# Kernel tuning notes

Hardware: AMD Instinct MI355X
Metric: run time of the kernel (lower is better)

## Reference

```python
import jax, jax.numpy as jnp
import numpy as np

B, F, H, OUT, S = 32768, 256, 128, 64, 6
RELAX, EPS, BN_EPS = 1.5, 1e-05, 1e-05
SQRT_HALF = 0.7071067811865476


def _bn(h, g, b):
    # training-mode BatchNorm1d: biased batch statistics over dim 0
    m = h.mean(axis=0)
    v = h.var(axis=0)
    return (h - m) * jax.lax.rsqrt(v + BN_EPS) * g + b


def _tfrm(x, W, g, b, glu_act=True):
    h = _bn(x @ W, g, b)
    if glu_act:
        d = h.shape[1] // 2
        h = h[:, :d] * jax.nn.sigmoid(h[:, d:])
    return h


def setup_inputs() -> dict:
    key = jax.random.key(0)
    ks = jax.random.split(key, 6)
    f32 = jnp.float32
    return {
        "x": jax.random.normal(ks[0], (B, F), f32),
        "enc_g": jnp.ones((F,), f32), "enc_b": jnp.zeros((F,), f32),
        "W1": jax.random.normal(ks[1], (F, 2 * H), f32) * 0.05,
        "g1": jnp.ones((2 * H,), f32), "b1": jnp.zeros((2 * H,), f32),
        "W2": jax.random.normal(ks[2], (H, 2 * H), f32) * 0.05,
        "g2": jnp.ones((2 * H,), f32), "b2": jnp.zeros((2 * H,), f32),
        "W3": jax.random.normal(ks[3], (S, H, 2 * H), f32) * 0.05,
        "g3": jnp.ones((S, 2 * H), f32), "b3": jnp.zeros((S, 2 * H), f32),
        "W4": jax.random.normal(ks[4], (S, H, 2 * H), f32) * 0.05,
        "g4": jnp.ones((S, 2 * H), f32), "b4": jnp.zeros((S, 2 * H), f32),
        "Wc": jax.random.normal(ks[5], (S - 1, OUT, F), f32) * 0.05,
        "gc": jnp.ones((S - 1, F), f32), "bc": jnp.zeros((S - 1, F), f32),
    }


def reference(x, enc_g, enc_b, W1, g1, b1, W2, g2, b2, W3, g3, b3,
              W4, g4, b4, Wc, gc, bc):
    x = _bn(x, enc_g, enc_b)                      # [B, F]
    masked = x
    compl = jnp.ones((x.shape[0], F), x.dtype)    # complementary aggregated mask
    agg_out, agg_entropy = [], []
    for ni in range(S):
        h = _tfrm(masked, W1, g1, b1)                             # [B, H]
        h = (_tfrm(h, W2, g2, b2) + h) * SQRT_HALF
        h = (_tfrm(h, W3[ni], g3[ni], b3[ni]) + h) * SQRT_HALF
        h = (_tfrm(h, W4[ni], g4[ni], b4[ni]) + h) * SQRT_HALF
        if ni > 0:
            # NOTE: source uses x (not h) here -- replicated faithfully
            agg_out.append(jax.nn.relu(x[:, :OUT]))
        fc = h[:, OUT:]                                           # [B, OUT]
        if ni < S - 1:
            coef = _tfrm(fc, Wc[ni], gc[ni], bc[ni], glu_act=False)  # [B, F]
            mask_values = jax.nn.softmax(coef * compl, axis=1)
            compl = compl * (RELAX - mask_values)
            agg_entropy.append(
                jnp.mean(jnp.sum(-mask_values * jnp.log(mask_values + EPS), axis=1))
                / (S - 1))
            masked = mask_values * x
    out = jnp.sum(jnp.stack(agg_out, axis=0), axis=0)   # [B, OUT]
    entropy = jnp.sum(jnp.stack(agg_entropy))           # scalar
    return (out, entropy)
```

## Files before the change

kernel.cpp:

```cpp
#include <hip/hip_runtime.h>
#include <math.h>

#define BSZ   32768
#define FDIM  256
#define HDIM  128
#define OUTD  64
#define SQRT_HALF 0.70710678118654752f
#define BN_EPS 1e-5f
#define SM_EPS 1e-5f
#define INV_B (1.0f / 32768.0f)
#define NCPY  8
#define SLOT  (NCPY * 512)

typedef __attribute__((ext_vector_type(8))) short bf16x8;
typedef __attribute__((ext_vector_type(4))) float f32x4;

__device__ __forceinline__ float b2f(unsigned short u) {
    return __uint_as_float(((unsigned int)u) << 16);
}
__device__ __forceinline__ unsigned short f2b(float f) {
    unsigned int u = __float_as_uint(f);
    u += 0x7fff + ((u >> 16) & 1);
    return (unsigned short)(u >> 16);
}

__device__ __forceinline__ void async16(const void* g, void* l) {
    __builtin_amdgcn_global_load_lds(
        (const __attribute__((address_space(1))) void*)(uintptr_t)g,
        (__attribute__((address_space(3))) void*)(unsigned int)(uintptr_t)l,
        16, 0, 0);
}

__device__ inline float waveMaxAll(float v) {
#pragma unroll
    for (int m = 32; m > 0; m >>= 1) v = fmaxf(v, __shfl_xor(v, m, 64));
    return v;
}
__device__ inline float waveSumAll(float v) {
#pragma unroll
    for (int m = 32; m > 0; m >>= 1) v += __shfl_xor(v, m, 64);
    return v;
}

__global__ __launch_bounds__(256) void prep_w(
    const float* __restrict__ W1, const float* __restrict__ W2,
    const float* __restrict__ W3, const float* __restrict__ W4,
    const float* __restrict__ Wc,
    unsigned short* __restrict__ W1t, unsigned short* __restrict__ W2t,
    unsigned short* __restrict__ W3t, unsigned short* __restrict__ W4t,
    unsigned short* __restrict__ Wct)
{
    const int m = blockIdx.x, kz = blockIdx.y, n = threadIdx.x;
    const float* src; unsigned short* dst; int K;
    if (m == 0)      { src = W1;                        dst = W1t;               K = 256; }
    else if (m == 1) { src = W2;                        dst = W2t;               K = 128; }
    else if (m < 7)  { int i = m - 2;  src = W3 + (size_t)i * 128 * 256; dst = W3t + (size_t)i * 32768; K = 128; }
    else if (m < 12) { int i = m - 7;  src = W4 + (size_t)i * 128 * 256; dst = W4t + (size_t)i * 32768; K = 128; }
    else             { int i = m - 12; src = Wc + (size_t)i * 64 * 256;  dst = Wct + (size_t)i * 16384; K = 64; }
    const int k0 = kz * 32;
    if (k0 >= K) return;
    for (int k = k0; k < k0 + 32; ++k)
        dst[(size_t)n * K + k] = f2b(src[(size_t)k * 256 + n]);
}

__global__ __launch_bounds__(256) void colstats(const float* __restrict__ X,
                                                float* __restrict__ st0) {
    __shared__ float red[4][512];
    const int sub = threadIdx.x >> 6;
    const int c4  = (threadIdx.x & 63) << 2;
    float s[4] = {0.f, 0.f, 0.f, 0.f}, q[4] = {0.f, 0.f, 0.f, 0.f};
#pragma unroll 8
    for (int i = 0; i < 32; ++i) {
        const int row = blockIdx.x * 128 + i * 4 + sub;
        float4 v = *(const float4*)(X + (size_t)row * 256 + c4);
        s[0] += v.x; q[0] += v.x * v.x;
        s[1] += v.y; q[1] += v.y * v.y;
        s[2] += v.z; q[2] += v.z * v.z;
        s[3] += v.w; q[3] += v.w * v.w;
    }
#pragma unroll
    for (int e = 0; e < 4; ++e) {
        red[sub][c4 + e] = s[e];
        red[sub][256 + c4 + e] = q[e];
    }
    __syncthreads();
    const int t = threadIdx.x;
    const int cp = (blockIdx.x & (NCPY - 1)) * 512;
    float sS = red[0][t] + red[1][t] + red[2][t] + red[3][t];
    float sQ = red[0][256 + t] + red[1][256 + t] + red[2][256 + t] + red[3][256 + t];
    atomicAdd(&st0[cp + t], sS);
    atomicAdd(&st0[cp + 256 + t], sQ);
}

__global__ __launch_bounds__(256) void norm_x(const float* __restrict__ x,
                                              const float* __restrict__ st0,
                                              const float* __restrict__ g,
                                              const float* __restrict__ b,
                                              unsigned short* __restrict__ xb,
                                              float* __restrict__ out) {
    const int i4 = blockIdx.x * 256 + threadIdx.x;
    const int row = i4 >> 6, c4 = (i4 & 63) << 2;
    float4 xv = *(const float4*)(x + (size_t)row * 256 + c4);
    float sS[4] = {0.f, 0.f, 0.f, 0.f}, sQ[4] = {0.f, 0.f, 0.f, 0.f};
#pragma unroll
    for (int cp = 0; cp < NCPY; ++cp) {
        float4 a = *(const float4*)&st0[cp * 512 + c4];
        float4 q = *(const float4*)&st0[cp * 512 + 256 + c4];
        sS[0] += a.x; sS[1] += a.y; sS[2] += a.z; sS[3] += a.w;
        sQ[0] += q.x; sQ[1] += q.y; sQ[2] += q.z; sQ[3] += q.w;
    }
    float4 gv = *(const float4*)&g[c4];
    float4 bv = *(const float4*)&b[c4];
    const float* xp = (const float*)&xv;
    const float* gp = (const float*)&gv; const float* bp = (const float*)&bv;
    float n[4];
    ushort4 ob;
    unsigned short* obp = (unsigned short*)&ob;
#pragma unroll
    for (int e = 0; e < 4; ++e) {
        float mean = sS[e] * INV_B;
        float var  = sQ[e] * INV_B - mean * mean;
        float sc   = gp[e] * rsqrtf(var + BN_EPS);
        float sh   = bp[e] - mean * sc;
        n[e] = xp[e] * sc + sh;
        obp[e] = f2b(n[e]);
    }
    *(ushort4*)(xb + (size_t)row * 256 + c4) = ob;
    if (c4 < OUTD) {
        float4 ov = make_float4(5.0f * fmaxf(n[0], 0.f), 5.0f * fmaxf(n[1], 0.f),
                                5.0f * fmaxf(n[2], 0.f), 5.0f * fmaxf(n[3], 0.f));
        *(float4*)(out + (size_t)row * OUTD + c4) = ov;
    }
}

__device__ __forceinline__ void gemm_epilogue(
    f32x4 (&acc)[4][4], int row0, int wave, int lane, int tid, int bcp,
    float* redS, float* redQ,
    unsigned short* __restrict__ Pout, float* __restrict__ statsOut)
{
    const int fm = lane & 15;
    const int orow = row0 + (lane >> 4) * 4;
    const int ocol = wave * 64 + fm;
#pragma unroll
    for (int i = 0; i < 4; ++i)
#pragma unroll
        for (int j = 0; j < 4; ++j)
#pragma unroll
            for (int r = 0; r < 4; ++r)
                Pout[(size_t)(orow + i * 16 + r) * 256 + (ocol + j * 16)] = f2b(acc[i][j][r]);

#pragma unroll
    for (int j = 0; j < 4; ++j) {
        float s = 0.f, q = 0.f;
#pragma unroll
        for (int i = 0; i < 4; ++i)
#pragma unroll
            for (int r = 0; r < 4; ++r) {
                float v = acc[i][j][r];
                s += v; q += v * v;
            }
        s += __shfl_xor(s, 16, 64); s += __shfl_xor(s, 32, 64);
        q += __shfl_xor(q, 16, 64); q += __shfl_xor(q, 32, 64);
        if (lane < 16) {
            redS[wave * 64 + j * 16 + lane] = s;
            redQ[wave * 64 + j * 16 + lane] = q;
        }
    }
    __syncthreads();
    atomicAdd(&statsOut[bcp + tid], redS[tid]);
    atomicAdd(&statsOut[bcp + 256 + tid], redQ[tid]);
}

__global__ __launch_bounds__(256) void gemm_bf16(
    const unsigned short* __restrict__ A,
    const unsigned short* __restrict__ Wt, int K,
    unsigned short* __restrict__ P,
    float* __restrict__ statsOut)
{
    __shared__ short As[64 * 32];
    __shared__ short Bs[256 * 32];
    __shared__ float redS[256], redQ[256];

    const int tid  = threadIdx.x;
    const int wave = tid >> 6;
    const int lane = tid & 63;
    const int row0 = blockIdx.x * 64;
    const int bcp  = (blockIdx.x & (NCPY - 1)) * 512;

    const int sr = lane >> 2;
    const int sc = (lane & 3) * 8;
    const int fm = lane & 15;
    const int fq = (lane >> 4) * 8;

    f32x4 acc[4][4];
#pragma unroll
    for (int i = 0; i < 4; ++i)
#pragma unroll
        for (int j = 0; j < 4; ++j)
            acc[i][j] = (f32x4){0.f, 0.f, 0.f, 0.f};

    for (int k0 = 0; k0 < K; k0 += 32) {
        async16(A + (size_t)(row0 + wave * 16 + sr) * K + k0 + sc,
                (void*)(As + wave * 512 + lane * 8));
#pragma unroll
        for (int t = 0; t < 4; ++t) {
            const int wr = wave * 64 + t * 16 + sr;
            async16(Wt + (size_t)wr * K + k0 + sc,
                    (void*)(Bs + (wave * 4 + t) * 512 + lane * 8));
        }
        __syncthreads();

        bf16x8 af[4], bfr[4];
#pragma unroll
        for (int i = 0; i < 4; ++i)
            af[i] = *(const bf16x8*)(As + (i * 16 + fm) * 32 + fq);
#pragma unroll
        for (int j = 0; j < 4; ++j)
            bfr[j] = *(const bf16x8*)(Bs + (wave * 64 + j * 16 + fm) * 32 + fq);
#pragma unroll
        for (int i = 0; i < 4; ++i)
#pragma unroll
            for (int j = 0; j < 4; ++j)
                acc[i][j] = __builtin_amdgcn_mfma_f32_16x16x32_bf16(af[i], bfr[j], acc[i][j], 0, 0, 0);
        __syncthreads();
    }

    gemm_epilogue(acc, row0, wave, lane, tid, bcp, redS, redQ, P, statsOut);
}

template <bool RES, bool WRITE_H>
__global__ __launch_bounds__(256) void gemm_glu(
    const unsigned short* __restrict__ Pprev,
    const float* __restrict__ pstats,
    const float* __restrict__ pg,
    const float* __restrict__ pb,
    const unsigned short* __restrict__ res,
    int colOff,
    const unsigned short* __restrict__ Wt, int K,
    unsigned short* __restrict__ Pout,
    float* __restrict__ statsOut,
    unsigned short* __restrict__ hOut)
{
    __shared__ short As[64 * 32];
    __shared__ short Bs[256 * 32];
    __shared__ float redS[256], redQ[256];
    __shared__ float tScA[128], tShA[128], tScG[128], tShG[128];

    const int tid  = threadIdx.x;
    const int wave = tid >> 6;
    const int lane = tid & 63;
    const int row0 = blockIdx.x * 64;
    const int bcp  = (blockIdx.x & (NCPY - 1)) * 512;

    if (tid < K) {
        const int ch = colOff + tid;
        const int cg = ch + 128;
        float sA = 0.f, qA = 0.f, sG = 0.f, qG = 0.f;
#pragma unroll
        for (int cp = 0; cp < NCPY; ++cp) {
            const float* p = pstats + cp * 512;
            sA += p[ch]; qA += p[256 + ch];
            sG += p[cg]; qG += p[256 + cg];
        }
        float ma = sA * INV_B, va = qA * INV_B - ma * ma;
        float scA = pg[ch] * rsqrtf(va + BN_EPS);
        tScA[tid] = scA; tShA[tid] = pb[ch] - ma * scA;
        float mg = sG * INV_B, vg = qG * INV_B - mg * mg;
        float scG = pg[cg] * rsqrtf(vg + BN_EPS);
        tScG[tid] = scG; tShG[tid] = pb[cg] - mg * scG;
    }
    __syncthreads();

    const int sr = lane >> 2;
    const int sc = (lane & 3) * 8;
    const int ar = tid >> 2;
    const int ac = (tid & 3) * 8;
    const int fm = lane & 15;
    const int fq = (lane >> 4) * 8;

    f32x4 acc[4][4];
#pragma unroll
    for (int i = 0; i < 4; ++i)
#pragma unroll
        for (int j = 0; j < 4; ++j)
            acc[i][j] = (f32x4){0.f, 0.f, 0.f, 0.f};

    for (int k0 = 0; k0 < K; k0 += 32) {
#pragma unroll
        for (int t = 0; t < 4; ++t) {
            const int wr = wave * 64 + t * 16 + sr;
            async16(Wt + (size_t)wr * K + k0 + sc,
                    (void*)(Bs + (wave * 4 + t) * 512 + lane * 8));
        }

        {
            const int kk = k0 + ac;
            const size_t grow = (size_t)(row0 + ar);

            bf16x8 lo = *(const bf16x8*)(Pprev + grow * 256 + colOff + kk);
            bf16x8 hi = *(const bf16x8*)(Pprev + grow * 256 + colOff + kk + 128);
            bf16x8 rv;
            if (RES) rv = *(const bf16x8*)(res + grow * 128 + kk);

            float4 a0 = *(const float4*)&tScA[kk], a1 = *(const float4*)&tScA[kk + 4];
            float4 h0 = *(const float4*)&tShA[kk], h1 = *(const float4*)&tShA[kk + 4];
            float4 g0 = *(const float4*)&tScG[kk], g1 = *(const float4*)&tScG[kk + 4];
            float4 s0 = *(const float4*)&tShG[kk], s1 = *(const float4*)&tShG[kk + 4];
            float scA[8] = {a0.x, a0.y, a0.z, a0.w, a1.x, a1.y, a1.z, a1.w};
            float shA[8] = {h0.x, h0.y, h0.z, h0.w, h1.x, h1.y, h1.z, h1.w};
            float scG[8] = {g0.x, g0.y, g0.z, g0.w, g1.x, g1.y, g1.z, g1.w};
            float shG[8] = {s0.x, s0.y, s0.z, s0.w, s1.x, s1.y, s1.z, s1.w};

            bf16x8 o8;
#pragma unroll
            for (int e = 0; e < 8; ++e) {
                float na = b2f((unsigned short)lo[e]) * scA[e] + shA[e];
                float ng = b2f((unsigned short)hi[e]) * scG[e] + shG[e];
                float v = na * (1.0f / (1.0f + __expf(-ng)));
                if (RES) v = (v + b2f((unsigned short)rv[e])) * SQRT_HALF;
                o8[e] = (short)f2b(v);
            }
            *(bf16x8*)(As + ar * 32 + ac) = o8;
            if (WRITE_H)
                *(bf16x8*)(hOut + grow * 128 + kk) = o8;
        }
        __syncthreads();

        bf16x8 af[4], bfr[4];
#pragma unroll
        for (int i = 0; i < 4; ++i)
            af[i] = *(const bf16x8*)(As + (i * 16 + fm) * 32 + fq);
#pragma unroll
        for (int j = 0; j < 4; ++j)
            bfr[j] = *(const bf16x8*)(Bs + (wave * 64 + j * 16 + fm) * 32 + fq);
#pragma unroll
        for (int i = 0; i < 4; ++i)
#pragma unroll
            for (int j = 0; j < 4; ++j)
                acc[i][j] = __builtin_amdgcn_mfma_f32_16x16x32_bf16(af[i], bfr[j], acc[i][j], 0, 0, 0);
        __syncthreads();
    }

    gemm_epilogue(acc, row0, wave, lane, tid, bcp, redS, redQ, Pout, statsOut);
}

template <int MODE>
__global__ __launch_bounds__(256) void coef_mask(const unsigned short* __restrict__ Pc,
                                                 const float* __restrict__ stats,
                                                 const float* __restrict__ gc,
                                                 const float* __restrict__ bc,
                                                 const unsigned short* __restrict__ xb,
                                                 unsigned short* __restrict__ cmpl,
                                                 unsigned short* __restrict__ masked,
                                                 float* __restrict__ ent) {
    const int w    = threadIdx.x >> 6;
    const int lane = threadIdx.x & 63;
    const int row  = blockIdx.x * 4 + w;
    const int c    = lane << 2;
    __shared__ float went[4];

    float sS[4] = {0.f, 0.f, 0.f, 0.f}, sQ[4] = {0.f, 0.f, 0.f, 0.f};
#pragma unroll
    for (int cp = 0; cp < NCPY; ++cp) {
        float4 a = *(const float4*)&stats[cp * 512 + c];
        float4 q = *(const float4*)&stats[cp * 512 + 256 + c];
        sS[0] += a.x; sS[1] += a.y; sS[2] += a.z; sS[3] += a.w;
        sQ[0] += q.x; sQ[1] += q.y; sQ[2] += q.z; sQ[3] += q.w;
    }
    float4 gv = *(const float4*)&gc[c];
    float4 bv = *(const float4*)&bc[c];
    const float* gvv = (const float*)&gv; const float* bvv = (const float*)&bv;

    float scl[4], shf[4];
#pragma unroll
    for (int e = 0; e < 4; ++e) {
        float mean = sS[e] * INV_B, var = sQ[e] * INV_B - mean * mean;
        scl[e] = gvv[e] * rsqrtf(var + BN_EPS);
        shf[e] = bvv[e] - mean * scl[e];
    }

    const size_t idx = (size_t)row * 256 + c;
    ushort4 pu = *(const ushort4*)(Pc + idx);
    const unsigned short* puv = (const unsigned short*)&pu;

    float cl[4] = {1.f, 1.f, 1.f, 1.f};
    if (MODE != 0) {
        ushort4 cu = *(const ushort4*)(cmpl + idx);
        const unsigned short* cuv = (const unsigned short*)&cu;
#pragma unroll
        for (int e = 0; e < 4; ++e) cl[e] = b2f(cuv[e]);
    }

    float l[4];
#pragma unroll
    for (int e = 0; e < 4; ++e) l[e] = (b2f(puv[e]) * scl[e] + shf[e]) * cl[e];

    float mx = waveMaxAll(fmaxf(fmaxf(l[0], l[1]), fmaxf(l[2], l[3])));
    float e0 = __expf(l[0] - mx), e1 = __expf(l[1] - mx),
          e2 = __expf(l[2] - mx), e3 = __expf(l[3] - mx);
    float inv = 1.0f / waveSumAll(e0 + e1 + e2 + e3);

    float m[4] = {e0 * inv, e1 * inv, e2 * inv, e3 * inv};

    float et = -m[0] * __logf(m[0] + SM_EPS) - m[1] * __logf(m[1] + SM_EPS)
             - m[2] * __logf(m[2] + SM_EPS) - m[3] * __logf(m[3] + SM_EPS);
    et = waveSumAll(et);
    if (lane == 0) went[w] = et;
    __syncthreads();
    if (threadIdx.x == 0) {
        float v = went[0] + went[1] + went[2] + went[3];
        atomicAdd(&ent[(blockIdx.x & 255) << 5], v * (INV_B * 0.2f));
    }

    if (MODE != 2) {
        ushort4 xu = *(const ushort4*)(xb + idx);
        const unsigned short* xuv = (const unsigned short*)&xu;
        ushort4 co, mo;
        unsigned short* cop = (unsigned short*)&co;
        unsigned short* mop = (unsigned short*)&mo;
#pragma unroll
        for (int e = 0; e < 4; ++e) {
            cop[e] = f2b(cl[e] * (1.5f - m[e]));
            mop[e] = f2b(m[e] * b2f(xuv[e]));
        }
        *(ushort4*)&cmpl[idx]   = co;
        *(ushort4*)&masked[idx] = mo;
    }
}

__global__ __launch_bounds__(64) void write_ent(const float* __restrict__ ent,
                                                float* __restrict__ dst) {
    const int lane = threadIdx.x;
    float v = 0.f;
#pragma unroll
    for (int i = 0; i < 4; ++i) v += ent[(lane + 64 * i) << 5];
    v = waveSumAll(v);
    if (lane == 0) dst[0] = v;
}

extern "C" void kernel_launch(void* const* d_in, const int* in_sizes, int n_in,
                              void* d_out, int out_size, void* d_ws, size_t ws_size,
                              hipStream_t stream) {
    const float* x     = (const float*)d_in[0];
    const float* enc_g = (const float*)d_in[1];
    const float* enc_b = (const float*)d_in[2];
    const float* W1 = (const float*)d_in[3];
    const float* g1 = (const float*)d_in[4];
    const float* b1 = (const float*)d_in[5];
    const float* W2 = (const float*)d_in[6];
    const float* g2 = (const float*)d_in[7];
    const float* b2 = (const float*)d_in[8];
    const float* W3 = (const float*)d_in[9];
    const float* g3 = (const float*)d_in[10];
    const float* b3 = (const float*)d_in[11];
    const float* W4 = (const float*)d_in[12];
    const float* g4 = (const float*)d_in[13];
    const float* b4 = (const float*)d_in[14];
    const float* Wc = (const float*)d_in[15];
    const float* gc = (const float*)d_in[16];
    const float* bc = (const float*)d_in[17];
    float* out = (float*)d_out;

    const size_t NBF = (size_t)BSZ * FDIM;
    const size_t NBH = (size_t)BSZ * HDIM;

    unsigned short* xb     = (unsigned short*)d_ws;
    unsigned short* masked = xb + NBF;
    unsigned short* Pb1    = masked + NBF;
    unsigned short* h1     = Pb1 + NBF;
    unsigned short* h2     = h1 + NBH;
    unsigned short* h3     = h2 + NBH;
    unsigned short* cmpl   = h3 + NBH;
    unsigned short* W1t    = cmpl + NBF;
    unsigned short* W2t    = W1t + 65536;
    unsigned short* W3t    = W2t + 32768;
    unsigned short* W4t    = W3t + 163840;
    unsigned short* Wct    = W4t + 163840;
    float* stats = (float*)(Wct + 81920);
    float* ent   = stats + 26 * SLOT;

    unsigned short* Pb2 = masked;

    hipMemsetAsync(stats, 0, (26 * SLOT + 256 * 32) * sizeof(float), stream);

    prep_w<<<dim3(17, 8), 256, 0, stream>>>(W1, W2, W3, W4, Wc, W1t, W2t, W3t, W4t, Wct);
    colstats<<<256, 256, 0, stream>>>(x, stats);
    norm_x<<<8192, 256, 0, stream>>>(x, stats, enc_g, enc_b, xb, out);

    for (int ni = 0; ni < 5; ++ni) {
        float* s1 = stats + (size_t)(1 + ni * 5 + 0) * SLOT;
        float* s2 = stats + (size_t)(1 + ni * 5 + 1) * SLOT;
        float* s3 = stats + (size_t)(1 + ni * 5 + 2) * SLOT;
        float* s4 = stats + (size_t)(1 + ni * 5 + 3) * SLOT;
        float* s5 = stats + (size_t)(1 + ni * 5 + 4) * SLOT;

        const unsigned short* in1 = (ni == 0) ? xb : masked;

        gemm_bf16<<<512, 256, 0, stream>>>(in1, W1t, 256, Pb1, s1);
        gemm_glu<false, true><<<512, 256, 0, stream>>>(
            Pb1, s1, g1, b1, nullptr, 0, W2t, 128, Pb2, s2, h1);
        gemm_glu<true, true><<<512, 256, 0, stream>>>(
            Pb2, s2, g2, b2, h1, 0, W3t + (size_t)ni * 32768, 128, Pb1, s3, h2);
        gemm_glu<true, true><<<512, 256, 0, stream>>>(
            Pb1, s3, g3 + ni * 256, b3 + ni * 256, h2, 0,
            W4t + (size_t)ni * 32768, 128, Pb2, s4, h3);
        gemm_glu<true, false><<<512, 256, 0, stream>>>(
            Pb2, s4, g4 + ni * 256, b4 + ni * 256, h3 + 64, 64,
            Wct + (size_t)ni * 16384, 64, Pb1, s5, nullptr);

        if (ni == 0)
            coef_mask<0><<<BSZ / 4, 256, 0, stream>>>(Pb1, s5, gc, bc, xb, cmpl, masked, ent);
        else if (ni < 4)
            coef_mask<1><<<BSZ / 4, 256, 0, stream>>>(Pb1, s5, gc + ni * 256, bc + ni * 256,
                                                      xb, cmpl, masked, ent);
        else
            coef_mask<2><<<BSZ / 4, 256, 0, stream>>>(Pb1, s5, gc + ni * 256, bc + ni * 256,
                                                      xb, cmpl, masked, ent);
    }

    write_ent<<<1, 64, 0, stream>>>(ent, out + (size_t)BSZ * OUTD);
}
```

Measured before the change: 613.4 us.

## Double-buffer LDS tiles in GEMM kernels to overlap loads with MFMA

```diff
diff --git a/kernel.cpp b/kernel.cpp
--- a/kernel.cpp
+++ b/kernel.cpp
@@ -177,8 +177,8 @@
     unsigned short* __restrict__ P,
     float* __restrict__ statsOut)
 {
-    __shared__ short As[64 * 32];
-    __shared__ short Bs[256 * 32];
+    __shared__ short As[2][64 * 32];
+    __shared__ short Bs[2][256 * 32];
     __shared__ float redS[256], redQ[256];
 
     const int tid  = threadIdx.x;
@@ -199,24 +199,40 @@
         for (int j = 0; j < 4; ++j)
             acc[i][j] = (f32x4){0.f, 0.f, 0.f, 0.f};
 
-    for (int k0 = 0; k0 < K; k0 += 32) {
-        async16(A + (size_t)(row0 + wave * 16 + sr) * K + k0 + sc,
-                (void*)(As + wave * 512 + lane * 8));
+    {
+        async16(A + (size_t)(row0 + wave * 16 + sr) * K + sc,
+                (void*)(&As[0][wave * 512 + lane * 8]));
 #pragma unroll
         for (int t = 0; t < 4; ++t) {
             const int wr = wave * 64 + t * 16 + sr;
-            async16(Wt + (size_t)wr * K + k0 + sc,
-                    (void*)(Bs + (wave * 4 + t) * 512 + lane * 8));
-        }
-        __syncthreads();
+            async16(Wt + (size_t)wr * K + sc,
+                    (void*)(&Bs[0][(wave * 4 + t) * 512 + lane * 8]));
+        }
+    }
+    __syncthreads();
+
+    const int nch = K >> 5;
+    for (int c = 0; c < nch; ++c) {
+        const int buf = c & 1;
+        if (c + 1 < nch) {
+            const int k1 = (c + 1) * 32;
+            async16(A + (size_t)(row0 + wave * 16 + sr) * K + k1 + sc,
+                    (void*)(&As[buf ^ 1][wave * 512 + lane * 8]));
+#pragma unroll
+            for (int t = 0; t < 4; ++t) {
+                const int wr = wave * 64 + t * 16 + sr;
+                async16(Wt + (size_t)wr * K + k1 + sc,
+                        (void*)(&Bs[buf ^ 1][(wave * 4 + t) * 512 + lane * 8]));
+            }
+        }
 
         bf16x8 af[4], bfr[4];
 #pragma unroll
         for (int i = 0; i < 4; ++i)
-            af[i] = *(const bf16x8*)(As + (i * 16 + fm) * 32 + fq);
+            af[i] = *(const bf16x8*)(&As[buf][(i * 16 + fm) * 32 + fq]);
 #pragma unroll
         for (int j = 0; j < 4; ++j)
-            bfr[j] = *(const bf16x8*)(Bs + (wave * 64 + j * 16 + fm) * 32 + fq);
+            bfr[j] = *(const bf16x8*)(&Bs[buf][(wave * 64 + j * 16 + fm) * 32 + fq]);
 #pragma unroll
         for (int i = 0; i < 4; ++i)
 #pragma unroll
@@ -241,8 +257,8 @@
     float* __restrict__ statsOut,
     unsigned short* __restrict__ hOut)
 {
-    __shared__ short As[64 * 32];
-    __shared__ short Bs[256 * 32];
+    __shared__ short As[2][64 * 32];
+    __shared__ short Bs[2][256 * 32];
     __shared__ float redS[256], redQ[256];
     __shared__ float tScA[128], tShA[128], tScG[128], tShG[128];
 
@@ -277,6 +293,7 @@
     const int ac = (tid & 3) * 8;
     const int fm = lane & 15;
     const int fq = (lane >> 4) * 8;
+    const size_t grow = (size_t)(row0 + ar);
 
     f32x4 acc[4][4];
 #pragma unroll
@@ -285,59 +302,75 @@
         for (int j = 0; j < 4; ++j)
             acc[i][j] = (f32x4){0.f, 0.f, 0.f, 0.f};
 
-    for (int k0 = 0; k0 < K; k0 += 32) {
+    auto gluA = [&](int k0, int buf, bf16x8 lo, bf16x8 hi, bf16x8 rv) {
+        const int kk = k0 + ac;
+        float4 a0 = *(const float4*)&tScA[kk], a1 = *(const float4*)&tScA[kk + 4];
+        float4 h0 = *(const float4*)&tShA[kk], h1 = *(const float4*)&tShA[kk + 4];
+        float4 g0 = *(const float4*)&tScG[kk], g1 = *(const float4*)&tScG[kk + 4];
+        float4 s0 = *(const float4*)&tShG[kk], s1 = *(const float4*)&tShG[kk + 4];
+        float scA[8] = {a0.x, a0.y, a0.z, a0.w, a1.x, a1.y, a1.z, a1.w};
+        float shA[8] = {h0.x, h0.y, h0.z, h0.w, h1.x, h1.y, h1.z, h1.w};
+        float scG[8] = {g0.x, g0.y, g0.z, g0.w, g1.x, g1.y, g1.z, g1.w};
+        float shG[8] = {s0.x, s0.y, s0.z, s0.w, s1.x, s1.y, s1.z, s1.w};
+        bf16x8 o8;
+#pragma unroll
+        for (int e = 0; e < 8; ++e) {
+            float na = b2f((unsigned short)lo[e]) * scA[e] + shA[e];
+            float ng = b2f((unsigned short)hi[e]) * scG[e] + shG[e];
+            float v = na * (1.0f / (1.0f + __expf(-ng)));
+            if (RES) v = (v + b2f((unsigned short)rv[e])) * SQRT_HALF;
+            o8[e] = (short)f2b(v);
+        }
+        *(bf16x8*)(&As[buf][ar * 32 + ac]) = o8;
+        if (WRITE_H)
+            *(bf16x8*)(hOut + grow * 128 + kk) = o8;
+    };
+    auto issueB = [&](int k0, int buf) {
 #pragma unroll
         for (int t = 0; t < 4; ++t) {
             const int wr = wave * 64 + t * 16 + sr;
             async16(Wt + (size_t)wr * K + k0 + sc,
-                    (void*)(Bs + (wave * 4 + t) * 512 + lane * 8));
-        }
-
-        {
-            const int kk = k0 + ac;
-            const size_t grow = (size_t)(row0 + ar);
-
-            bf16x8 lo = *(const bf16x8*)(Pprev + grow * 256 + colOff + kk);
-            bf16x8 hi = *(const bf16x8*)(Pprev + grow * 256 + colOff + kk + 128);
-            bf16x8 rv;
-            if (RES) rv = *(const bf16x8*)(res + grow * 128 + kk);
-
-            float4 a0 = *(const float4*)&tScA[kk], a1 = *(const float4*)&tScA[kk + 4];
-            float4 h0 = *(const float4*)&tShA[kk], h1 = *(const float4*)&tShA[kk + 4];
-            float4 g0 = *(const float4*)&tScG[kk], g1 = *(const float4*)&tScG[kk + 4];
-            float4 s0 = *(const float4*)&tShG[kk], s1 = *(const float4*)&tShG[kk + 4];
-            float scA[8] = {a0.x, a0.y, a0.z, a0.w, a1.x, a1.y, a1.z, a1.w};
-            float shA[8] = {h0.x, h0.y, h0.z, h0.w, h1.x, h1.y, h1.z, h1.w};
-            float scG[8] = {g0.x, g0.y, g0.z, g0.w, g1.x, g1.y, g1.z, g1.w};
-            float shG[8] = {s0.x, s0.y, s0.z, s0.w, s1.x, s1.y, s1.z, s1.w};
-
-            bf16x8 o8;
-#pragma unroll
-            for (int e = 0; e < 8; ++e) {
-                float na = b2f((unsigned short)lo[e]) * scA[e] + shA[e];
-                float ng = b2f((unsigned short)hi[e]) * scG[e] + shG[e];
-                float v = na * (1.0f / (1.0f + __expf(-ng)));
-                if (RES) v = (v + b2f((unsigned short)rv[e])) * SQRT_HALF;
-                o8[e] = (short)f2b(v);
-            }
-            *(bf16x8*)(As + ar * 32 + ac) = o8;
-            if (WRITE_H)
-                *(bf16x8*)(hOut + grow * 128 + kk) = o8;
-        }
-        __syncthreads();
+                    (void*)(&Bs[buf][(wave * 4 + t) * 512 + lane * 8]));
+        }
+    };
+
+    {
+        bf16x8 lo = *(const bf16x8*)(Pprev + grow * 256 + colOff + ac);
+        bf16x8 hi = *(const bf16x8*)(Pprev + grow * 256 + colOff + ac + 128);
+        bf16x8 rv{};
+        if (RES) rv = *(const bf16x8*)(res + grow * 128 + ac);
+        issueB(0, 0);
+        gluA(0, 0, lo, hi, rv);
+    }
+    __syncthreads();
+
+    const int nch = K >> 5;
+    for (int c = 0; c < nch; ++c) {
+        const int buf = c & 1;
+        bf16x8 lo{}, hi{}, rv{};
+        const int k1 = (c + 1) * 32;
+        if (c + 1 < nch) {
+            lo = *(const bf16x8*)(Pprev + grow * 256 + colOff + k1 + ac);
+            hi = *(const bf16x8*)(Pprev + grow * 256 + colOff + k1 + ac + 128);
+            if (RES) rv = *(const bf16x8*)(res + grow * 128 + k1 + ac);
+            issueB(k1, buf ^ 1);
+        }
 
         bf16x8 af[4], bfr[4];
 #pragma unroll
         for (int i = 0; i < 4; ++i)
-            af[i] = *(const bf16x8*)(As + (i * 16 + fm) * 32 + fq);
+            af[i] = *(const bf16x8*)(&As[buf][(i * 16 + fm) * 32 + fq]);
 #pragma unroll
         for (int j = 0; j < 4; ++j)
-            bfr[j] = *(const bf16x8*)(Bs + (wave * 64 + j * 16 + fm) * 32 + fq);
+            bfr[j] = *(const bf16x8*)(&Bs[buf][(wave * 64 + j * 16 + fm) * 32 + fq]);
 #pragma unroll
         for (int i = 0; i < 4; ++i)
 #pragma unroll
             for (int j = 0; j < 4; ++j)
                 acc[i][j] = __builtin_amdgcn_mfma_f32_16x16x32_bf16(af[i], bfr[j], acc[i][j], 0, 0, 0);
+
+        if (c + 1 < nch)
+            gluA(k1, buf ^ 1, lo, hi, rv);
         __syncthreads();
     }
 
```

Result: no change. 618.2 us (+0.8%).

## Fuse softmax mask computation into the next step's first GEMM prologue

Applied to the files above, without the earlier changes.

```diff
diff --git a/kernel.cpp b/kernel.cpp
--- a/kernel.cpp
+++ b/kernel.cpp
@@ -31,11 +31,6 @@
         16, 0, 0);
 }
 
-__device__ inline float waveMaxAll(float v) {
-#pragma unroll
-    for (int m = 32; m > 0; m >>= 1) v = fmaxf(v, __shfl_xor(v, m, 64));
-    return v;
-}
 __device__ inline float waveSumAll(float v) {
 #pragma unroll
     for (int m = 32; m > 0; m >>= 1) v += __shfl_xor(v, m, 64);
@@ -86,10 +81,9 @@
     __syncthreads();
     const int t = threadIdx.x;
     const int cp = (blockIdx.x & (NCPY - 1)) * 512;
-    float sS = red[0][t] + red[1][t] + red[2][t] + red[3][t];
-    float sQ = red[0][256 + t] + red[1][256 + t] + red[2][256 + t] + red[3][256 + t];
-    atomicAdd(&st0[cp + t], sS);
-    atomicAdd(&st0[cp + 256 + t], sQ);
+    atomicAdd(&st0[cp + t], red[0][t] + red[1][t] + red[2][t] + red[3][t]);
+    atomicAdd(&st0[cp + 256 + t],
+              red[0][256 + t] + red[1][256 + t] + red[2][256 + t] + red[3][256 + t]);
 }
 
 __global__ __launch_bounds__(256) void norm_x(const float* __restrict__ x,
@@ -201,22 +195,22 @@
 
     for (int k0 = 0; k0 < K; k0 += 32) {
         async16(A + (size_t)(row0 + wave * 16 + sr) * K + k0 + sc,
-                (void*)(As + wave * 512 + lane * 8));
+                (void*)(&As[wave * 512 + lane * 8]));
 #pragma unroll
         for (int t = 0; t < 4; ++t) {
             const int wr = wave * 64 + t * 16 + sr;
             async16(Wt + (size_t)wr * K + k0 + sc,
-                    (void*)(Bs + (wave * 4 + t) * 512 + lane * 8));
+                    (void*)(&Bs[(wave * 4 + t) * 512 + lane * 8]));
         }
         __syncthreads();
 
         bf16x8 af[4], bfr[4];
 #pragma unroll
         for (int i = 0; i < 4; ++i)
-            af[i] = *(const bf16x8*)(As + (i * 16 + fm) * 32 + fq);
+            af[i] = *(const bf16x8*)(&As[(i * 16 + fm) * 32 + fq]);
 #pragma unroll
         for (int j = 0; j < 4; ++j)
-            bfr[j] = *(const bf16x8*)(Bs + (wave * 64 + j * 16 + fm) * 32 + fq);
+            bfr[j] = *(const bf16x8*)(&Bs[(wave * 64 + j * 16 + fm) * 32 + fq]);
 #pragma unroll
         for (int i = 0; i < 4; ++i)
 #pragma unroll
@@ -226,6 +220,167 @@
     }
 
     gemm_epilogue(acc, row0, wave, lane, tid, bcp, redS, redQ, P, statsOut);
+}
+
+template <bool FIRST>
+__global__ __launch_bounds__(256) void gemm_coef(
+    const unsigned short* __restrict__ Pc,
+    const float* __restrict__ cstats,
+    const float* __restrict__ gcc, const float* __restrict__ bcc,
+    const unsigned short* __restrict__ xb,
+    unsigned short* __restrict__ cmpl,
+    const unsigned short* __restrict__ Wt,
+    unsigned short* __restrict__ Pout,
+    float* __restrict__ statsOut,
+    float* __restrict__ ent)
+{
+    __shared__ short Am[8][64 * 32];
+    __shared__ short Bs[256 * 32];
+    __shared__ float redS[256], redQ[256];
+    __shared__ float tScl[256], tShf[256];
+    __shared__ float blockEnt;
+
+    const int tid  = threadIdx.x;
+    const int wave = tid >> 6;
+    const int lane = tid & 63;
+    const int row0 = blockIdx.x * 64;
+    const int bcp  = (blockIdx.x & (NCPY - 1)) * 512;
+
+    {
+        float sS = 0.f, sQ = 0.f;
+#pragma unroll
+        for (int cp = 0; cp < NCPY; ++cp) {
+            sS += cstats[cp * 512 + tid];
+            sQ += cstats[cp * 512 + 256 + tid];
+        }
+        float mean = sS * INV_B, var = sQ * INV_B - mean * mean;
+        float sc = gcc[tid] * rsqrtf(var + BN_EPS);
+        tScl[tid] = sc; tShf[tid] = bcc[tid] - mean * sc;
+    }
+    if (tid == 0) blockEnt = 0.f;
+    __syncthreads();
+
+    {
+        const int row = tid >> 2, q = tid & 3;
+        const size_t rbase = (size_t)(row0 + row) * 256;
+        const unsigned short* prow = Pc + rbase;
+        const unsigned short* xrow = xb + rbase;
+        unsigned short* crow = cmpl + rbase;
+
+        float lv[8][8];
+        float mx = -3e38f;
+#pragma unroll
+        for (int b = 0; b < 8; ++b) {
+            const int c0 = q * 8 + b * 32;
+            bf16x8 p = *(const bf16x8*)(prow + c0);
+            float cl[8];
+            if (!FIRST) {
+                bf16x8 cu = *(const bf16x8*)(crow + c0);
+#pragma unroll
+                for (int e = 0; e < 8; ++e) cl[e] = b2f((unsigned short)cu[e]);
+            } else {
+#pragma unroll
+                for (int e = 0; e < 8; ++e) cl[e] = 1.f;
+            }
+            float4 t0 = *(const float4*)&tScl[c0], t1 = *(const float4*)&tScl[c0 + 4];
+            float4 f0 = *(const float4*)&tShf[c0], f1 = *(const float4*)&tShf[c0 + 4];
+            float scl[8] = {t0.x, t0.y, t0.z, t0.w, t1.x, t1.y, t1.z, t1.w};
+            float shf[8] = {f0.x, f0.y, f0.z, f0.w, f1.x, f1.y, f1.z, f1.w};
+#pragma unroll
+            for (int e = 0; e < 8; ++e) {
+                float l = (b2f((unsigned short)p[e]) * scl[e] + shf[e]) * cl[e];
+                lv[b][e] = l;
+                mx = fmaxf(mx, l);
+            }
+        }
+        mx = fmaxf(mx, __shfl_xor(mx, 1, 64));
+        mx = fmaxf(mx, __shfl_xor(mx, 2, 64));
+
+        float s = 0.f;
+#pragma unroll
+        for (int b = 0; b < 8; ++b)
+#pragma unroll
+            for (int e = 0; e < 8; ++e) {
+                float ev = __expf(lv[b][e] - mx);
+                lv[b][e] = ev;
+                s += ev;
+            }
+        s += __shfl_xor(s, 1, 64);
+        s += __shfl_xor(s, 2, 64);
+        const float inv = 1.0f / s;
+
+        float entAcc = 0.f;
+#pragma unroll
+        for (int b = 0; b < 8; ++b) {
+            const int c0 = q * 8 + b * 32;
+            float cl[8];
+            if (!FIRST) {
+                bf16x8 cu = *(const bf16x8*)(crow + c0);
+#pragma unroll
+                for (int e = 0; e < 8; ++e) cl[e] = b2f((unsigned short)cu[e]);
+            } else {
+#pragma unroll
+                for (int e = 0; e < 8; ++e) cl[e] = 1.f;
+            }
+            bf16x8 xu = *(const bf16x8*)(xrow + c0);
+            bf16x8 co, mo;
+#pragma unroll
+            for (int e = 0; e < 8; ++e) {
+                float m = lv[b][e] * inv;
+                entAcc += -m * __logf(m + SM_EPS);
+                co[e] = (short)f2b(cl[e] * (1.5f - m));
+                mo[e] = (short)f2b(m * b2f((unsigned short)xu[e]));
+            }
+            *(bf16x8*)(crow + c0) = co;
+            *(bf16x8*)(&Am[b][row * 32 + q * 8]) = mo;
+        }
+        entAcc += __shfl_xor(entAcc, 1, 64);
+        entAcc += __shfl_xor(entAcc, 2, 64);
+        if (q == 0) atomicAdd(&blockEnt, entAcc);
+    }
+    __syncthreads();
+    if (tid == 0)
+        atomicAdd(&ent[(blockIdx.x & 255) << 5], blockEnt * (INV_B * 0.2f));
+
+    const int sr = lane >> 2;
+    const int sc = (lane & 3) * 8;
+    const int fm = lane & 15;
+    const int fq = (lane >> 4) * 8;
+
+    f32x4 acc[4][4];
+#pragma unroll
+    for (int i = 0; i < 4; ++i)
+#pragma unroll
+        for (int j = 0; j < 4; ++j)
+            acc[i][j] = (f32x4){0.f, 0.f, 0.f, 0.f};
+
+#pragma unroll 1
+    for (int c = 0; c < 8; ++c) {
+        const int k0 = c * 32;
+#pragma unroll
+        for (int t = 0; t < 4; ++t) {
+            const int wr = wave * 64 + t * 16 + sr;
+            async16(Wt + (size_t)wr * 256 + k0 + sc,
+                    (void*)(&Bs[(wave * 4 + t) * 512 + lane * 8]));
+        }
+        __syncthreads();
+
+        bf16x8 af[4], bfr[4];
+#pragma unroll
+        for (int i = 0; i < 4; ++i)
+            af[i] = *(const bf16x8*)(&Am[c][(i * 16 + fm) * 32 + fq]);
+#pragma unroll
+        for (int j = 0; j < 4; ++j)
+            bfr[j] = *(const bf16x8*)(&Bs[(wave * 64 + j * 16 + fm) * 32 + fq]);
+#pragma unroll
+        for (int i = 0; i < 4; ++i)
+#pragma unroll
+            for (int j = 0; j < 4; ++j)
+                acc[i][j] = __builtin_amdgcn_mfma_f32_16x16x32_bf16(af[i], bfr[j], acc[i][j], 0, 0, 0);
+        __syncthreads();
+    }
+
+    gemm_epilogue(acc, row0, wave, lane, tid, bcp, redS, redQ, Pout, statsOut);
 }
 
 template <bool RES, bool WRITE_H>
@@ -290,16 +445,15 @@
         for (int t = 0; t < 4; ++t) {
             const int wr = wave * 64 + t * 16 + sr;
             async16(Wt + (size_t)wr * K + k0 + sc,
-                    (void*)(Bs + (wave * 4 + t) * 512 + lane * 8));
-        }
-
+                    (void*)(&Bs[(wave * 4 + t) * 512 + lane * 8]));
+        }
         {
             const int kk = k0 + ac;
             const size_t grow = (size_t)(row0 + ar);
 
             bf16x8 lo = *(const bf16x8*)(Pprev + grow * 256 + colOff + kk);
             bf16x8 hi = *(const bf16x8*)(Pprev + grow * 256 + colOff + kk + 128);
-            bf16x8 rv;
+            bf16x8 rv{};
             if (RES) rv = *(const bf16x8*)(res + grow * 128 + kk);
 
             float4 a0 = *(const float4*)&tScA[kk], a1 = *(const float4*)&tScA[kk + 4];
@@ -320,7 +474,7 @@
                 if (RES) v = (v + b2f((unsigned short)rv[e])) * SQRT_HALF;
                 o8[e] = (short)f2b(v);
             }
-            *(bf16x8*)(As + ar * 32 + ac) = o8;
+            *(bf16x8*)(&As[ar * 32 + ac]) = o8;
             if (WRITE_H)
                 *(bf16x8*)(hOut + grow * 128 + kk) = o8;
         }
@@ -329,10 +483,10 @@
         bf16x8 af[4], bfr[4];
 #pragma unroll
         for (int i = 0; i < 4; ++i)
-            af[i] = *(const bf16x8*)(As + (i * 16 + fm) * 32 + fq);
+            af[i] = *(const bf16x8*)(&As[(i * 16 + fm) * 32 + fq]);
 #pragma unroll
         for (int j = 0; j < 4; ++j)
-            bfr[j] = *(const bf16x8*)(Bs + (wave * 64 + j * 16 + fm) * 32 + fq);
+            bfr[j] = *(const bf16x8*)(&Bs[(wave * 64 + j * 16 + fm) * 32 + fq]);
 #pragma unroll
         for (int i = 0; i < 4; ++i)
 #pragma unroll
@@ -344,15 +498,12 @@
     gemm_epilogue(acc, row0, wave, lane, tid, bcp, redS, redQ, Pout, statsOut);
 }
 
-template <int MODE>
-__global__ __launch_bounds__(256) void coef_mask(const unsigned short* __restrict__ Pc,
-                                                 const float* __restrict__ stats,
-                                                 const float* __restrict__ gc,
-                                                 const float* __restrict__ bc,
-                                                 const unsigned short* __restrict__ xb,
-                                                 unsigned short* __restrict__ cmpl,
-                                                 unsigned short* __restrict__ masked,
-                                                 float* __restrict__ ent) {
+__global__ __launch_bounds__(256) void coef_ent(const unsigned short* __restrict__ Pc,
+                                                const float* __restrict__ stats,
+                                                const float* __restrict__ gc,
+                                                const float* __restrict__ bc,
+                                                const unsigned short* __restrict__ cmpl,
+                                                float* __restrict__ ent) {
     const int w    = threadIdx.x >> 6;
     const int lane = threadIdx.x & 63;
     const int row  = blockIdx.x * 4 + w;
@@ -381,50 +532,31 @@
 
     const size_t idx = (size_t)row * 256 + c;
     ushort4 pu = *(const ushort4*)(Pc + idx);
+    ushort4 cu = *(const ushort4*)(cmpl + idx);
     const unsigned short* puv = (const unsigned short*)&pu;
-
-    float cl[4] = {1.f, 1.f, 1.f, 1.f};
-    if (MODE != 0) {
-        ushort4 cu = *(const ushort4*)(cmpl + idx);
-        const unsigned short* cuv = (const unsigned short*)&cu;
-#pragma unroll
-        for (int e = 0; e < 4; ++e) cl[e] = b2f(cuv[e]);
-    }
+    const unsigned short* cuv = (const unsigned short*)&cu;
 
     float l[4];
 #pragma unroll
-    for (int e = 0; e < 4; ++e) l[e] = (b2f(puv[e]) * scl[e] + shf[e]) * cl[e];
-
-    float mx = waveMaxAll(fmaxf(fmaxf(l[0], l[1]), fmaxf(l[2], l[3])));
+    for (int e = 0; e < 4; ++e)
+        l[e] = (b2f(puv[e]) * scl[e] + shf[e]) * b2f(cuv[e]);
+
+    float mx = fmaxf(fmaxf(l[0], l[1]), fmaxf(l[2], l[3]));
+#pragma unroll
+    for (int m = 32; m > 0; m >>= 1) mx = fmaxf(mx, __shfl_xor(mx, m, 64));
     float e0 = __expf(l[0] - mx), e1 = __expf(l[1] - mx),
           e2 = __expf(l[2] - mx), e3 = __expf(l[3] - mx);
     float inv = 1.0f / waveSumAll(e0 + e1 + e2 + e3);
 
-    float m[4] = {e0 * inv, e1 * inv, e2 * inv, e3 * inv};
-
-    float et = -m[0] * __logf(m[0] + SM_EPS) - m[1] * __logf(m[1] + SM_EPS)
-             - m[2] * __logf(m[2] + SM_EPS) - m[3] * __logf(m[3] + SM_EPS);
+    float m0 = e0 * inv, m1 = e1 * inv, m2 = e2 * inv, m3 = e3 * inv;
+    float et = -m0 * __logf(m0 + SM_EPS) - m1 * __logf(m1 + SM_EPS)
+             - m2 * __logf(m2 + SM_EPS) - m3 * __logf(m3 + SM_EPS);
     et = waveSumAll(et);
     if (lane == 0) went[w] = et;
     __syncthreads();
     if (threadIdx.x == 0) {
         float v = went[0] + went[1] + went[2] + went[3];
         atomicAdd(&ent[(blockIdx.x & 255) << 5], v * (INV_B * 0.2f));
-    }
-
-    if (MODE != 2) {
-        ushort4 xu = *(const ushort4*)(xb + idx);
-        const unsigned short* xuv = (const unsigned short*)&xu;
-        ushort4 co, mo;
-        unsigned short* cop = (unsigned short*)&co;
-        unsigned short* mop = (unsigned short*)&mo;
-#pragma unroll
-        for (int e = 0; e < 4; ++e) {
-            cop[e] = f2b(cl[e] * (1.5f - m[e]));
-            mop[e] = f2b(m[e] * b2f(xuv[e]));
-        }
-        *(ushort4*)&cmpl[idx]   = co;
-        *(ushort4*)&masked[idx] = mo;
     }
 }
 
@@ -465,8 +597,8 @@
     const size_t NBH = (size_t)BSZ * HDIM;
 
     unsigned short* xb     = (unsigned short*)d_ws;
-    unsigned short* masked = xb + NBF;
-    unsigned short* Pb1    = masked + NBF;
+    unsigned short* Pb2    = xb + NBF;
+    unsigned short* Pb1    = Pb2 + NBF;
     unsigned short* h1     = Pb1 + NBF;
     unsigned short* h2     = h1 + NBH;
     unsigned short* h3     = h2 + NBH;
@@ -479,8 +611,6 @@
     float* stats = (float*)(Wct + 81920);
     float* ent   = stats + 26 * SLOT;
 
-    unsigned short* Pb2 = masked;
-
     hipMemsetAsync(stats, 0, (26 * SLOT + 256 * 32) * sizeof(float), stream);
 
     prep_w<<<dim3(17, 8), 256, 0, stream>>>(W1, W2, W3, W4, Wc, W1t, W2t, W3t, W4t, Wct);
@@ -494,9 +624,19 @@
         float* s4 = stats + (size_t)(1 + ni * 5 + 3) * SLOT;
         float* s5 = stats + (size_t)(1 + ni * 5 + 4) * SLOT;
 
-        const unsigned short* in1 = (ni == 0) ? xb : masked;
-
-        gemm_bf16<<<512, 256, 0, stream>>>(in1, W1t, 256, Pb1, s1);
+        if (ni == 0) {
+            gemm_bf16<<<512, 256, 0, stream>>>(xb, W1t, 256, Pb1, s1);
+        } else {
+            float* s5p = stats + (size_t)(1 + (ni - 1) * 5 + 4) * SLOT;
+            const float* gp = gc + (ni - 1) * 256;
+            const float* bp = bc + (ni - 1) * 256;
+            if (ni == 1)
+                gemm_coef<true><<<512, 256, 0, stream>>>(Pb1, s5p, gp, bp, xb, cmpl,
+                                                         W1t, Pb1, s1, ent);
+            else
+                gemm_coef<false><<<512, 256, 0, stream>>>(Pb1, s5p, gp, bp, xb, cmpl,
+                                                          W1t, Pb1, s1, ent);
+        }
         gemm_glu<false, true><<<512, 256, 0, stream>>>(
             Pb1, s1, g1, b1, nullptr, 0, W2t, 128, Pb2, s2, h1);
         gemm_glu<true, true><<<512, 256, 0, stream>>>(
@@ -507,16 +647,9 @@
         gemm_glu<true, false><<<512, 256, 0, stream>>>(
             Pb2, s4, g4 + ni * 256, b4 + ni * 256, h3 + 64, 64,
             Wct + (size_t)ni * 16384, 64, Pb1, s5, nullptr);
-
-        if (ni == 0)
-            coef_mask<0><<<BSZ / 4, 256, 0, stream>>>(Pb1, s5, gc, bc, xb, cmpl, masked, ent);
-        else if (ni < 4)
-            coef_mask<1><<<BSZ / 4, 256, 0, stream>>>(Pb1, s5, gc + ni * 256, bc + ni * 256,
-                                                      xb, cmpl, masked, ent);
-        else
-            coef_mask<2><<<BSZ / 4, 256, 0, stream>>>(Pb1, s5, gc + ni * 256, bc + ni * 256,
-                                                      xb, cmpl, masked, ent);
-    }
-
+    }
+
+    coef_ent<<<BSZ / 4, 256, 0, stream>>>(Pb1, stats + (size_t)(1 + 4 * 5 + 4) * SLOT,
+                                          gc + 4 * 256, bc + 4 * 256, cmpl, ent);
     write_ent<<<1, 64, 0, stream>>>(ent, out + (size_t)BSZ * OUTD);
 }
```

New measurement: 632.2 us. 3.1% more time.
